# Performance work log

Hardware: AMD Instinct MI355X
Metric: run time of the kernel (lower is better)

## Reference

```python
import jax, jax.numpy as jnp
import numpy as np

DIM = 576
SCALE = DIM ** -0.5  # num_heads=1 -> head_dim = dim
EPS = 1e-5


def _layernorm(x, g, b):
    mu = jnp.mean(x, axis=-1, keepdims=True)
    var = jnp.mean(jnp.square(x - mu), axis=-1, keepdims=True)
    return (x - mu) * jax.lax.rsqrt(var + EPS) * g + b


def _cross(x, y, lnx_g, lnx_b, lny_g, lny_b, lnz_g, lnz_b, Wq, Wk, Wv, Wp, bp):
    # x, y: [B, N, C]; attends y (query) over x (key/value), residual from normed x
    xn = _layernorm(x, lnx_g, lnx_b)
    yn = _layernorm(y, lny_g, lny_b)
    q = jnp.einsum('bnd,od->bno', yn, Wq)
    k = jnp.einsum('bnd,od->bno', xn, Wk)
    v = jnp.einsum('bnd,od->bno', xn, Wv)
    attn = jax.nn.sigmoid(jnp.einsum('bqd,bkd->bqk', q, k) * SCALE)  # [B,N,N]
    o = jnp.einsum('bqk,bkd->bqd', attn, v)
    o = jnp.einsum('bnd,od->bno', o, Wp) + bp + xn
    return _layernorm(o, lnz_g, lnz_b)


def setup_inputs() -> dict:
    key = jax.random.key(0)
    ks = jax.random.split(key, 16)
    B, N, C = 8, 1024, DIM
    s = C ** -0.5
    inp = {
        'image_t': jax.random.normal(ks[0], (B, N, C), jnp.float32),
        'aolp_t': jax.random.normal(ks[1], (B, N, C), jnp.float32),
        'dolp_t': jax.random.normal(ks[2], (B, N, C), jnp.float32),
        # 6 Cross blocks, params stacked along axis 0
        'lnx_g': jnp.ones((6, C), jnp.float32),
        'lnx_b': jnp.zeros((6, C), jnp.float32),
        'lny_g': jnp.ones((6, C), jnp.float32),
        'lny_b': jnp.zeros((6, C), jnp.float32),
        'lnz_g': jnp.ones((6, C), jnp.float32),
        'lnz_b': jnp.zeros((6, C), jnp.float32),
        'Wq': jax.random.normal(ks[3], (6, C, C), jnp.float32) * s,
        'Wk': jax.random.normal(ks[4], (6, C, C), jnp.float32) * s,
        'Wv': jax.random.normal(ks[5], (6, C, C), jnp.float32) * s,
        'Wp': jax.random.normal(ks[6], (6, C, C), jnp.float32) * s,
        'bp': jnp.zeros((6, C), jnp.float32),
        'Wf': jax.random.normal(ks[7], (C, 6 * C), jnp.float32) * (6 * C) ** -0.5,
        'bf': jnp.zeros((C,), jnp.float32),
    }
    return inp


def reference(image_t, aolp_t, dolp_t, lnx_g, lnx_b, lny_g, lny_b, lnz_g, lnz_b,
              Wq, Wk, Wv, Wp, bp, Wf, bf):
    # pair order matches Fusion_T: (img,aolp),(img,dolp),(aolp,img),(aolp,dolp),(dolp,img),(dolp,aolp)
    xs = jnp.stack([image_t, image_t, aolp_t, aolp_t, dolp_t, dolp_t])  # [6,B,N,C]
    ys = jnp.stack([aolp_t, dolp_t, image_t, dolp_t, image_t, aolp_t])
    outs = jax.vmap(_cross)(xs, ys, lnx_g, lnx_b, lny_g, lny_b, lnz_g, lnz_b,
                            Wq, Wk, Wv, Wp, bp)  # [6,B,N,C]
    B, N, C = image_t.shape
    concat = jnp.transpose(outs, (1, 2, 0, 3)).reshape(B, N, 6 * C)
    fused = jnp.einsum('bnd,od->bno', concat, Wf) + bf
    return jax.nn.gelu(fused, approximate=False)
```

## Files before the change

kernel.cpp:

```cpp
#include <hip/hip_runtime.h>
#include <math.h>

#define LN_EPS 1e-5f

typedef short s8v __attribute__((ext_vector_type(8)));
typedef float f4v __attribute__((ext_vector_type(4)));

__device__ __forceinline__ short f2bf(float x) {
  union { float f; unsigned u; } v; v.f = x;
  const unsigned r = v.u + 0x7fffu + ((v.u >> 16) & 1u);
  return (short)(r >> 16);
}
__device__ __forceinline__ float bf2f(short s) {
  union { unsigned u; float f; } v;
  v.u = ((unsigned)(unsigned short)s) << 16;
  return v.f;
}

__device__ __forceinline__ void gld16(const void* g, void* l) {
  __builtin_amdgcn_global_load_lds(
      (const __attribute__((address_space(1))) void*)g,
      (__attribute__((address_space(3))) void*)l, 16, 0, 0);
}

enum { EP_SPLIT = 0, EP_SIG, EP_RES, EP_BIAS, EP_ACC, EP_ACCGELU };

template <int EP, int WC>
__global__ __launch_bounds__(128 * WC) void gemmk(
    const short* Ah, const short* Al, const short* Bh, const short* Bl,
    short* Ch, short* Cl, float* Cf, const float* bias, const short* resH,
    const short* resL, float* out2, int pnCnt, int pmCnt, int lda, int ldb,
    int ldc, int K, long sA, long sB, long sC, float scale) {
  constexpr int BM = 128, BN = 64 * WC, T = 128 * WC;
  constexpr int RA = (BM * 128) / (T * 16);
  constexpr int RB = (BN * 128) / (T * 16);
  __shared__ short lds[(2 * BM + 2 * BN) * 64];
  short* AsH = lds;
  short* AsL = lds + BM * 64;
  short* BsH = lds + 2 * BM * 64;
  short* BsL = lds + 2 * BM * 64 + BN * 64;

  const int tid = threadIdx.x;
  const int lane = tid & 63;
  const int wave = tid >> 6;
  const int wr = wave / WC;
  const int wc = wave % WC;
  const int half = lane >> 4;
  const int l15 = lane & 15;

  const int chunk = gridDim.x >> 3;
  const int l = ((int)blockIdx.x & 7) * chunk + ((int)blockIdx.x >> 3);
  const int pn = l % pnCnt;
  const int t1 = l / pnCnt;
  const int pm = t1 % pmCnt;
  const long zb = t1 / pmCnt;
  const int bm = pm * BM;
  const int bn = pn * BN;

  Ah += zb * sA; Al += zb * sA;
  Bh += zb * sB; Bl += zb * sB;

  f4v acc[4][4];
#pragma unroll
  for (int i = 0; i < 4; ++i)
#pragma unroll
    for (int j = 0; j < 4; ++j)
#pragma unroll
      for (int r = 0; r < 4; ++r) acc[i][j][r] = 0.f;

  for (int k0 = 0; k0 < K; k0 += 64) {
    __syncthreads();
#pragma unroll
    for (int t = 0; t < RA; ++t) {
      const int off = (t * T + tid) * 16;
      const int row = off >> 7;
      const int ke = ((((off >> 4) & 7) ^ (row & 7)) << 3);
      const long ga = (long)(bm + row) * lda + k0 + ke;
      gld16(Ah + ga, (char*)AsH + off);
      gld16(Al + ga, (char*)AsL + off);
    }
#pragma unroll
    for (int t = 0; t < RB; ++t) {
      const int off = (t * T + tid) * 16;
      const int row = off >> 7;
      const int ke = ((((off >> 4) & 7) ^ (row & 7)) << 3);
      const long gb = (long)(bn + row) * ldb + k0 + ke;
      gld16(Bh + gb, (char*)BsH + off);
      gld16(Bl + gb, (char*)BsL + off);
    }
    __syncthreads();

#pragma unroll
    for (int s = 0; s < 2; ++s) {
      s8v ah[4], al[4], bh[4], bl[4];
#pragma unroll
      for (int i = 0; i < 4; ++i) {
        const int r = wr * 64 + i * 16 + l15;
        const int ad = r * 64 + ((((s << 2) + half) ^ (r & 7)) << 3);
        ah[i] = *(const s8v*)&AsH[ad];
        al[i] = *(const s8v*)&AsL[ad];
      }
#pragma unroll
      for (int j = 0; j < 4; ++j) {
        const int c = wc * 64 + j * 16 + l15;
        const int bd = c * 64 + ((((s << 2) + half) ^ (c & 7)) << 3);
        bh[j] = *(const s8v*)&BsH[bd];
        bl[j] = *(const s8v*)&BsL[bd];
      }
#pragma unroll
      for (int i = 0; i < 4; ++i)
#pragma unroll
        for (int j = 0; j < 4; ++j) {
          acc[i][j] = __builtin_amdgcn_mfma_f32_16x16x32_bf16(ah[i], bh[j],
                                                              acc[i][j], 0, 0, 0);
          acc[i][j] = __builtin_amdgcn_mfma_f32_16x16x32_bf16(ah[i], bl[j],
                                                              acc[i][j], 0, 0, 0);
          acc[i][j] = __builtin_amdgcn_mfma_f32_16x16x32_bf16(al[i], bh[j],
                                                              acc[i][j], 0, 0, 0);
        }
    }
  }

#pragma unroll
  for (int i = 0; i < 4; ++i) {
#pragma unroll
    for (int r = 0; r < 4; ++r) {
      const int row = bm + wr * 64 + i * 16 + half * 4 + r;
#pragma unroll
      for (int j = 0; j < 4; ++j) {
        const int col = bn + wc * 64 + j * 16 + l15;
        float x = acc[i][j][r];
        if (EP == EP_SPLIT) {
          const long idx = zb * sC + (long)row * ldc + col;
          const short h = f2bf(x);
          Ch[idx] = h;
          Cl[idx] = f2bf(x - bf2f(h));
        } else if (EP == EP_SIG) {
          x = 1.f / (1.f + expf(-x * scale));
          const long idx = zb * sC + (long)row * ldc + col;
          const short h = f2bf(x);
          Ch[idx] = h;
          Cl[idx] = f2bf(x - bf2f(h));
        } else if (EP == EP_RES) {
          const long idx = (long)row * ldc + col;
          Cf[idx] = x + bias[col] + bf2f(resH[idx]) + bf2f(resL[idx]);
        } else if (EP == EP_BIAS) {
          const long idx = (long)row * ldc + col;
          Cf[idx] = x + bias[col];
        } else if (EP == EP_ACC) {
          const long idx = (long)row * ldc + col;
          Cf[idx] += x;
        } else if (EP == EP_ACCGELU) {
          const long idx = (long)row * ldc + col;
          const float sum = Cf[idx] + x;
          out2[idx] = 0.5f * sum * (1.f + erff(sum * 0.70710678118654752f));
        }
      }
    }
  }
}

__global__ __launch_bounds__(128, 4) void proj3k(
    const short* ynh, const short* ynl, const short* xnh, const short* xnl,
    const short* wqh, const short* wql, const short* wkh, const short* wkl,
    const short* wvh, const short* wvl, short* qh, short* ql, short* kh,
    short* kl, short* vth, short* vtl) {
  constexpr int T = 128, RA = 8, RB = 4;
  __shared__ short As[128 * 64];
  __shared__ short Bs[64 * 64];

  const int tid = threadIdx.x;
  const int lane = tid & 63;
  const int wr = tid >> 6;
  const int half = lane >> 4;
  const int l15 = lane & 15;

  const int chunk = gridDim.x >> 3;
  const int l = ((int)blockIdx.x & 7) * chunk + ((int)blockIdx.x >> 3);
  const int pn = l % 27;
  const int pm = l / 27;
  const int sel = pn / 9;
  const int bm = pm * 128;
  const int bn = (pn - sel * 9) * 64;

  const short* Ah = sel ? xnh : ynh;
  const short* Al = sel ? xnl : ynl;
  const short* Bh = sel == 0 ? wqh : (sel == 1 ? wkh : wvh);
  const short* Bl = sel == 0 ? wql : (sel == 1 ? wkl : wvl);

  f4v acc[4][4];
#pragma unroll
  for (int i = 0; i < 4; ++i)
#pragma unroll
    for (int j = 0; j < 4; ++j)
#pragma unroll
      for (int r = 0; r < 4; ++r) acc[i][j][r] = 0.f;

  for (int k0 = 0; k0 < 576; k0 += 32) {
    __syncthreads();
#pragma unroll
    for (int t = 0; t < RA; ++t) {
      const int off = (t * T + tid) * 16;
      const int row = off >> 7;
      const int c = ((off >> 4) & 7) ^ (row & 7);
      const short* src = (c & 4) ? Al : Ah;
      gld16(src + (long)(bm + row) * 576 + k0 + ((c & 3) << 3),
            (char*)As + off);
    }
#pragma unroll
    for (int t = 0; t < RB; ++t) {
      const int off = (t * T + tid) * 16;
      const int row = off >> 7;
      const int c = ((off >> 4) & 7) ^ (row & 7);
      const short* src = (c & 4) ? Bl : Bh;
      gld16(src + (long)(bn + row) * 576 + k0 + ((c & 3) << 3),
            (char*)Bs + off);
    }
    __syncthreads();

    s8v ah[4], al[4], bh[4], bl[4];
#pragma unroll
    for (int i = 0; i < 4; ++i) {
      const int r = wr * 64 + i * 16 + l15;
      const int s0 = r * 64 + ((half ^ (r & 7)) << 3);
      ah[i] = *(const s8v*)&As[s0];
      al[i] = *(const s8v*)&As[s0 ^ 32];
    }
#pragma unroll
    for (int j = 0; j < 4; ++j) {
      const int c2 = j * 16 + l15;
      const int s0 = c2 * 64 + ((half ^ (c2 & 7)) << 3);
      bh[j] = *(const s8v*)&Bs[s0];
      bl[j] = *(const s8v*)&Bs[s0 ^ 32];
    }
#pragma unroll
    for (int i = 0; i < 4; ++i)
#pragma unroll
      for (int j = 0; j < 4; ++j) {
        acc[i][j] = __builtin_amdgcn_mfma_f32_16x16x32_bf16(ah[i], bh[j],
                                                            acc[i][j], 0, 0, 0);
        acc[i][j] = __builtin_amdgcn_mfma_f32_16x16x32_bf16(ah[i], bl[j],
                                                            acc[i][j], 0, 0, 0);
        acc[i][j] = __builtin_amdgcn_mfma_f32_16x16x32_bf16(al[i], bh[j],
                                                            acc[i][j], 0, 0, 0);
      }
  }

#pragma unroll
  for (int i = 0; i < 4; ++i) {
#pragma unroll
    for (int r = 0; r < 4; ++r) {
      const int row = bm + wr * 64 + i * 16 + half * 4 + r;
#pragma unroll
      for (int j = 0; j < 4; ++j) {
        const int col = bn + j * 16 + l15;
        const float x = acc[i][j][r];
        const short h = f2bf(x);
        const short lo = f2bf(x - bf2f(h));
        if (sel == 2) {
          const long idx = ((long)(row >> 10) * 576 + col) * 1024 + (row & 1023);
          vth[idx] = h;
          vtl[idx] = lo;
        } else {
          const long idx = (long)row * 576 + col;
          short* oh = sel ? kh : qh;
          short* ol = sel ? kl : ql;
          oh[idx] = h;
          ol[idx] = lo;
        }
      }
    }
  }
}

__global__ __launch_bounds__(576) void ln576(const float* __restrict__ x,
                                             const float* __restrict__ g,
                                             const float* __restrict__ b,
                                             short* __restrict__ oh,
                                             short* __restrict__ ol) {
  __shared__ float red[2][9];
  __shared__ float mu_s, rs_s;
  const long row = blockIdx.x;
  const int t = threadIdx.x;
  const float v = x[row * 576 + t];
  float s = v, s2 = v * v;
#pragma unroll
  for (int off = 32; off > 0; off >>= 1) {
    s += __shfl_xor(s, off);
    s2 += __shfl_xor(s2, off);
  }
  if ((t & 63) == 0) {
    red[0][t >> 6] = s;
    red[1][t >> 6] = s2;
  }
  __syncthreads();
  if (t == 0) {
    float a = 0.f, a2 = 0.f;
#pragma unroll
    for (int i = 0; i < 9; ++i) {
      a += red[0][i];
      a2 += red[1][i];
    }
    const float mu = a * (1.f / 576.f);
    mu_s = mu;
    rs_s = rsqrtf(a2 * (1.f / 576.f) - mu * mu + LN_EPS);
  }
  __syncthreads();
  const float y = (v - mu_s) * rs_s * g[t] + b[t];
  const short h = f2bf(y);
  oh[row * 576 + t] = h;
  ol[row * 576 + t] = f2bf(y - bf2f(h));
}

__global__ __launch_bounds__(256) void splitk(const float* __restrict__ in,
                                              short* __restrict__ oh,
                                              short* __restrict__ ol, long n) {
  long i = (long)blockIdx.x * blockDim.x + threadIdx.x;
  const long stride = (long)gridDim.x * blockDim.x;
  for (; i < n; i += stride) {
    const float x = in[i];
    const short h = f2bf(x);
    oh[i] = h;
    ol[i] = f2bf(x - bf2f(h));
  }
}

extern "C" void kernel_launch(void* const* d_in, const int* in_sizes, int n_in,
                              void* d_out, int out_size, void* d_ws,
                              size_t ws_size, hipStream_t stream) {
  const float* img = (const float*)d_in[0];
  const float* aolp = (const float*)d_in[1];
  const float* dolp = (const float*)d_in[2];
  const float* lnx_g = (const float*)d_in[3];
  const float* lnx_b = (const float*)d_in[4];
  const float* lny_g = (const float*)d_in[5];
  const float* lny_b = (const float*)d_in[6];
  const float* lnz_g = (const float*)d_in[7];
  const float* lnz_b = (const float*)d_in[8];
  const float* Wq = (const float*)d_in[9];
  const float* Wk = (const float*)d_in[10];
  const float* Wv = (const float*)d_in[11];
  const float* Wp = (const float*)d_in[12];
  const float* bp = (const float*)d_in[13];
  const float* Wf = (const float*)d_in[14];
  const float* bf = (const float*)d_in[15];
  float* out = (float*)d_out;

  const long S = 8L * 1024 * 576;
  const long W = 6L * 576 * 576;
  char* p = (char*)d_ws;
  auto alloc = [&](long bytes) {
    char* r = p;
    p += (bytes + 255) & ~255L;
    return r;
  };
  short* xn_h = (short*)alloc(S * 2);
  short* xn_l = (short*)alloc(S * 2);
  short* yn_h = (short*)alloc(S * 2);
  short* yn_l = (short*)alloc(S * 2);
  short* q_h = (short*)alloc(S * 2);
  short* q_l = (short*)alloc(S * 2);
  short* k_h = (short*)alloc(S * 2);
  short* k_l = (short*)alloc(S * 2);
  short* vt_h = (short*)alloc(S * 2);
  short* vt_l = (short*)alloc(S * 2);
  short* attn_h = (short*)alloc(8L * 1024 * 1024 * 2 * 2);
  short* attn_l = attn_h + 8L * 1024 * 1024;
  float* t_f32 = (float*)attn_h;
  float* fused = (float*)alloc(S * 4);
  short* wq_h = (short*)alloc(W * 2);
  short* wq_l = (short*)alloc(W * 2);
  short* wk_h = (short*)alloc(W * 2);
  short* wk_l = (short*)alloc(W * 2);
  short* wv_h = (short*)alloc(W * 2);
  short* wv_l = (short*)alloc(W * 2);
  short* wp_h = (short*)alloc(W * 2);
  short* wp_l = (short*)alloc(W * 2);
  short* wf_h = (short*)alloc(W * 2);
  short* wf_l = (short*)alloc(W * 2);

  splitk<<<1024, 256, 0, stream>>>(Wq, wq_h, wq_l, W);
  splitk<<<1024, 256, 0, stream>>>(Wk, wk_h, wk_l, W);
  splitk<<<1024, 256, 0, stream>>>(Wv, wv_h, wv_l, W);
  splitk<<<1024, 256, 0, stream>>>(Wp, wp_h, wp_l, W);
  splitk<<<1024, 256, 0, stream>>>(Wf, wf_h, wf_l, W);

  const float* src[3] = {img, aolp, dolp};
  const int xi[6] = {0, 0, 1, 1, 2, 2};
  const int yi[6] = {1, 2, 0, 2, 0, 1};
  const float scale = 1.f / 24.f;

  const int nProj3 = 27 * 64;
  const int nScore = 8 * 8 * 8;
  const int nAV = 9 * 8 * 8;
  const int nN = 9 * 64;

  for (int z = 0; z < 6; ++z) {
    const long wo = (long)z * 576 * 576;
    ln576<<<8192, 576, 0, stream>>>(src[xi[z]], lnx_g + z * 576,
                                    lnx_b + z * 576, xn_h, xn_l);
    ln576<<<8192, 576, 0, stream>>>(src[yi[z]], lny_g + z * 576,
                                    lny_b + z * 576, yn_h, yn_l);
    proj3k<<<nProj3, 128, 0, stream>>>(
        yn_h, yn_l, xn_h, xn_l, wq_h + wo, wq_l + wo, wk_h + wo, wk_l + wo,
        wv_h + wo, wv_l + wo, q_h, q_l, k_h, k_l, vt_h, vt_l);
    gemmk<EP_SIG, 2><<<nScore, 256, 0, stream>>>(
        q_h, q_l, k_h, k_l, attn_h, attn_l, nullptr, nullptr, nullptr, nullptr,
        nullptr, 8, 8, 576, 576, 1024, 576, 1024L * 576, 1024L * 576,
        1024L * 1024, scale);
    gemmk<EP_SPLIT, 1><<<nAV, 128, 0, stream>>>(
        attn_h, attn_l, vt_h, vt_l, yn_h, yn_l, nullptr, nullptr, nullptr,
        nullptr, nullptr, 9, 8, 1024, 1024, 576, 1024, 1024L * 1024,
        576L * 1024, 1024L * 576, 0.f);
    gemmk<EP_RES, 1><<<nN, 128, 0, stream>>>(
        yn_h, yn_l, wp_h + wo, wp_l + wo, nullptr, nullptr, t_f32, bp + z * 576,
        xn_h, xn_l, nullptr, 9, 64, 576, 576, 576, 576, 0, 0, 0, 0.f);
    ln576<<<8192, 576, 0, stream>>>(t_f32, lnz_g + z * 576, lnz_b + z * 576,
                                    q_h, q_l);
    if (z == 0)
      gemmk<EP_BIAS, 1><<<nN, 128, 0, stream>>>(
          q_h, q_l, wf_h + z * 576, wf_l + z * 576, nullptr, nullptr, fused, bf,
          nullptr, nullptr, nullptr, 9, 64, 576, 3456, 576, 576, 0, 0, 0, 0.f);
    else if (z < 5)
      gemmk<EP_ACC, 1><<<nN, 128, 0, stream>>>(
          q_h, q_l, wf_h + z * 576, wf_l + z * 576, nullptr, nullptr, fused,
          nullptr, nullptr, nullptr, nullptr, 9, 64, 576, 3456, 576, 576, 0, 0,
          0, 0.f);
    else
      gemmk<EP_ACCGELU, 1><<<nN, 128, 0, stream>>>(
          q_h, q_l, wf_h + z * 576, wf_l + z * 576, nullptr, nullptr, fused,
          nullptr, nullptr, nullptr, out, 9, 64, 576, 3456, 576, 576, 0, 0, 0,
          0.f);
  }
}
```

Before: 2.008 ms.

## Double-buffer LDS tiles in GEMM kernels to overlap loads with MFMA

Both the generic GEMM kernel and the QKV projection kernel now keep two LDS buffers. Each iteration prefetches the next K-slice into the spare buffer while MFMAs run on the current one, so only one barrier per step remains. The generic GEMM also moves from separate hi/lo LDS arrays with a 64-wide K step to an interleaved hi/lo 32-wide K layout, matching the projection kernel. The cost is twice the LDS per block, which may reduce occupancy, and the projection kernel drops its occupancy hint of 4 blocks.

Result: faster. 1.895 ms (-5.7%).

```diff
diff --git a/kernel.cpp b/kernel.cpp
--- a/kernel.cpp
+++ b/kernel.cpp
@@ -34,11 +34,7 @@
   constexpr int BM = 128, BN = 64 * WC, T = 128 * WC;
   constexpr int RA = (BM * 128) / (T * 16);
   constexpr int RB = (BN * 128) / (T * 16);
-  __shared__ short lds[(2 * BM + 2 * BN) * 64];
-  short* AsH = lds;
-  short* AsL = lds + BM * 64;
-  short* BsH = lds + 2 * BM * 64;
-  short* BsL = lds + 2 * BM * 64 + BN * 64;
+  __shared__ short lds[2][(BM + BN) * 64];
 
   const int tid = threadIdx.x;
   const int lane = tid & 63;
@@ -60,65 +56,73 @@
   Ah += zb * sA; Al += zb * sA;
   Bh += zb * sB; Bl += zb * sB;
 
-  f4v acc[4][4];
-#pragma unroll
-  for (int i = 0; i < 4; ++i)
-#pragma unroll
-    for (int j = 0; j < 4; ++j)
-#pragma unroll
-      for (int r = 0; r < 4; ++r) acc[i][j][r] = 0.f;
-
-  for (int k0 = 0; k0 < K; k0 += 64) {
-    __syncthreads();
+  auto STAGE = [&](int b, int k0) {
+    short* As = lds[b];
+    short* Bs = lds[b] + BM * 64;
 #pragma unroll
     for (int t = 0; t < RA; ++t) {
       const int off = (t * T + tid) * 16;
       const int row = off >> 7;
-      const int ke = ((((off >> 4) & 7) ^ (row & 7)) << 3);
-      const long ga = (long)(bm + row) * lda + k0 + ke;
-      gld16(Ah + ga, (char*)AsH + off);
-      gld16(Al + ga, (char*)AsL + off);
+      const int c = ((off >> 4) & 7) ^ (row & 7);
+      const short* src = (c & 4) ? Al : Ah;
+      gld16(src + (long)(bm + row) * lda + k0 + ((c & 3) << 3),
+            (char*)As + off);
     }
 #pragma unroll
     for (int t = 0; t < RB; ++t) {
       const int off = (t * T + tid) * 16;
       const int row = off >> 7;
-      const int ke = ((((off >> 4) & 7) ^ (row & 7)) << 3);
-      const long gb = (long)(bn + row) * ldb + k0 + ke;
-      gld16(Bh + gb, (char*)BsH + off);
-      gld16(Bl + gb, (char*)BsL + off);
-    }
+      const int c = ((off >> 4) & 7) ^ (row & 7);
+      const short* src = (c & 4) ? Bl : Bh;
+      gld16(src + (long)(bn + row) * ldb + k0 + ((c & 3) << 3),
+            (char*)Bs + off);
+    }
+  };
+
+  f4v acc[4][4];
+#pragma unroll
+  for (int i = 0; i < 4; ++i)
+#pragma unroll
+    for (int j = 0; j < 4; ++j)
+#pragma unroll
+      for (int r = 0; r < 4; ++r) acc[i][j][r] = 0.f;
+
+  STAGE(0, 0);
+  __syncthreads();
+  int cur = 0;
+  const int nt = K >> 5;
+  for (int t = 0; t < nt; ++t) {
+    if (t + 1 < nt) STAGE(cur ^ 1, (t + 1) << 5);
+    const short* As = lds[cur];
+    const short* Bs = lds[cur] + BM * 64;
+    s8v ah[4], al[4], bh[4], bl[4];
+#pragma unroll
+    for (int i = 0; i < 4; ++i) {
+      const int r = wr * 64 + i * 16 + l15;
+      const int s0 = r * 64 + ((half ^ (r & 7)) << 3);
+      ah[i] = *(const s8v*)&As[s0];
+      al[i] = *(const s8v*)&As[s0 ^ 32];
+    }
+#pragma unroll
+    for (int j = 0; j < 4; ++j) {
+      const int c2 = wc * 64 + j * 16 + l15;
+      const int s0 = c2 * 64 + ((half ^ (c2 & 7)) << 3);
+      bh[j] = *(const s8v*)&Bs[s0];
+      bl[j] = *(const s8v*)&Bs[s0 ^ 32];
+    }
+#pragma unroll
+    for (int i = 0; i < 4; ++i)
+#pragma unroll
+      for (int j = 0; j < 4; ++j) {
+        acc[i][j] = __builtin_amdgcn_mfma_f32_16x16x32_bf16(ah[i], bh[j],
+                                                            acc[i][j], 0, 0, 0);
+        acc[i][j] = __builtin_amdgcn_mfma_f32_16x16x32_bf16(ah[i], bl[j],
+                                                            acc[i][j], 0, 0, 0);
+        acc[i][j] = __builtin_amdgcn_mfma_f32_16x16x32_bf16(al[i], bh[j],
+                                                            acc[i][j], 0, 0, 0);
+      }
     __syncthreads();
-
-#pragma unroll
-    for (int s = 0; s < 2; ++s) {
-      s8v ah[4], al[4], bh[4], bl[4];
-#pragma unroll
-      for (int i = 0; i < 4; ++i) {
-        const int r = wr * 64 + i * 16 + l15;
-        const int ad = r * 64 + ((((s << 2) + half) ^ (r & 7)) << 3);
-        ah[i] = *(const s8v*)&AsH[ad];
-        al[i] = *(const s8v*)&AsL[ad];
-      }
-#pragma unroll
-      for (int j = 0; j < 4; ++j) {
-        const int c = wc * 64 + j * 16 + l15;
-        const int bd = c * 64 + ((((s << 2) + half) ^ (c & 7)) << 3);
-        bh[j] = *(const s8v*)&BsH[bd];
-        bl[j] = *(const s8v*)&BsL[bd];
-      }
-#pragma unroll
-      for (int i = 0; i < 4; ++i)
-#pragma unroll
-        for (int j = 0; j < 4; ++j) {
-          acc[i][j] = __builtin_amdgcn_mfma_f32_16x16x32_bf16(ah[i], bh[j],
-                                                              acc[i][j], 0, 0, 0);
-          acc[i][j] = __builtin_amdgcn_mfma_f32_16x16x32_bf16(ah[i], bl[j],
-                                                              acc[i][j], 0, 0, 0);
-          acc[i][j] = __builtin_amdgcn_mfma_f32_16x16x32_bf16(al[i], bh[j],
-                                                              acc[i][j], 0, 0, 0);
-        }
-    }
+    cur ^= 1;
   }
 
 #pragma unroll
@@ -160,14 +164,13 @@
   }
 }
 
-__global__ __launch_bounds__(128, 4) void proj3k(
+__global__ __launch_bounds__(128) void proj3k(
     const short* ynh, const short* ynl, const short* xnh, const short* xnl,
     const short* wqh, const short* wql, const short* wkh, const short* wkl,
     const short* wvh, const short* wvl, short* qh, short* ql, short* kh,
     short* kl, short* vth, short* vtl) {
   constexpr int T = 128, RA = 8, RB = 4;
-  __shared__ short As[128 * 64];
-  __shared__ short Bs[64 * 64];
+  __shared__ short lds[2][(128 + 64) * 64];
 
   const int tid = threadIdx.x;
   const int lane = tid & 63;
@@ -188,16 +191,9 @@
   const short* Bh = sel == 0 ? wqh : (sel == 1 ? wkh : wvh);
   const short* Bl = sel == 0 ? wql : (sel == 1 ? wkl : wvl);
 
-  f4v acc[4][4];
-#pragma unroll
-  for (int i = 0; i < 4; ++i)
-#pragma unroll
-    for (int j = 0; j < 4; ++j)
-#pragma unroll
-      for (int r = 0; r < 4; ++r) acc[i][j][r] = 0.f;
-
-  for (int k0 = 0; k0 < 576; k0 += 32) {
-    __syncthreads();
+  auto STAGE = [&](int b, int k0) {
+    short* As = lds[b];
+    short* Bs = lds[b] + 128 * 64;
 #pragma unroll
     for (int t = 0; t < RA; ++t) {
       const int off = (t * T + tid) * 16;
@@ -216,8 +212,23 @@
       gld16(src + (long)(bn + row) * 576 + k0 + ((c & 3) << 3),
             (char*)Bs + off);
     }
-    __syncthreads();
-
+  };
+
+  f4v acc[4][4];
+#pragma unroll
+  for (int i = 0; i < 4; ++i)
+#pragma unroll
+    for (int j = 0; j < 4; ++j)
+#pragma unroll
+      for (int r = 0; r < 4; ++r) acc[i][j][r] = 0.f;
+
+  STAGE(0, 0);
+  __syncthreads();
+  int cur = 0;
+  for (int t = 0; t < 18; ++t) {
+    if (t + 1 < 18) STAGE(cur ^ 1, (t + 1) << 5);
+    const short* As = lds[cur];
+    const short* Bs = lds[cur] + 128 * 64;
     s8v ah[4], al[4], bh[4], bl[4];
 #pragma unroll
     for (int i = 0; i < 4; ++i) {
@@ -244,6 +255,8 @@
         acc[i][j] = __builtin_amdgcn_mfma_f32_16x16x32_bf16(al[i], bh[j],
                                                             acc[i][j], 0, 0, 0);
       }
+    __syncthreads();
+    cur ^= 1;
   }
 
 #pragma unroll
```
